# Kernel optimization log

Hardware: AMD Instinct MI355X
Metric: run time of the kernel (lower is better)

The kernel has to match this reference:

```python
import jax, jax.numpy as jnp
import numpy as np

EMBED_DIM = 1024
EXPAND_RATIO = 128  # head_dim; n_heads = EMBED_DIM // EXPAND_RATIO = 8
B, N = 4, 2048


def setup_inputs() -> dict:
    key = jax.random.key(0)
    ks = jax.random.split(key, 6)
    std = 0.02
    d = EMBED_DIM
    return {
        "x": jax.random.normal(ks[0], (B, N, d), dtype=jnp.float32),
        "Wq": jax.random.normal(ks[1], (d, d), dtype=jnp.float32) * std,
        "Wk": jax.random.normal(ks[2], (d, d), dtype=jnp.float32) * std,
        "Wv": jax.random.normal(ks[3], (d, d), dtype=jnp.float32) * std,
        "Wo": jax.random.normal(ks[4], (d, d), dtype=jnp.float32) * std,
        "norm_w": jnp.ones((d,), dtype=jnp.float32),
    }


def _rmsnorm(x, w, eps=1e-6):
    return x * jax.lax.rsqrt(jnp.mean(x * x, axis=-1, keepdims=True) + eps) * w


def _gla_scan(q, k, v, g):
    # q,k,v,g: [b, n, h, d]; state S: [b, h, d_k, d_v]
    b, n, h, d = q.shape
    qs, ks_, vs, gs = (jnp.moveaxis(t, 1, 0) for t in (q, k, v, g))  # [n,b,h,d]
    S0 = jnp.zeros((b, h, d, d), dtype=q.dtype)

    def step(S, inp):
        q_t, k_t, v_t, g_t = inp
        # S_t = diag(exp(g_t)) S_{t-1} + k_t^T v_t (gate on key dim)
        S = jnp.exp(g_t)[..., :, None] * S + k_t[..., :, None] * v_t[..., None, :]
        o_t = jnp.einsum('bhk,bhkv->bhv', q_t, S)
        return S, o_t

    _, outs = jax.lax.scan(step, S0, (qs, ks_, vs, gs))
    return jnp.moveaxis(outs, 0, 1)  # [b, n, h, d]


def reference(x, Wq, Wk, Wv, Wo, norm_w):
    b, n, D = x.shape
    hd = EXPAND_RATIO
    h = D // hd

    q = jax.nn.silu(x @ Wq.T)          # q_activation = silu
    f = jax.nn.sigmoid(x @ Wk.T)       # f = sigmoid(k_proj(x))
    log_f = jax.nn.log_sigmoid(f)      # faithful: logsigmoid applied to f (lower_bound=None path)
    k = 1.0 - f
    v = x @ Wv.T

    def split_heads(t):
        return t.reshape(b, n, h, hd)

    out = _gla_scan(split_heads(q), split_heads(k), split_heads(v), split_heads(log_f))
    out = out.reshape(b, n, D)
    out = _rmsnorm(out, norm_w)        # norm_pos='ogate', no output gate
    return out @ Wo.T
```

## Files before the change

### kernel.cpp

```cpp
#include <hip/hip_runtime.h>
#include <cstdint>
#include <cstddef>


typedef unsigned short u16;
using f32x4  = __attribute__((ext_vector_type(4))) float;
using bf16x8 = __attribute__((ext_vector_type(8))) short;

__device__ __forceinline__ float bf2f(u16 u) {
  union { unsigned int i; float f; } v; v.i = ((unsigned int)u) << 16; return v.f;
}
__device__ __forceinline__ u16 f2bf(float f) {
  union { float f; unsigned int i; } v; v.f = f;
  unsigned int r = v.i + 0x7fffu + ((v.i >> 16) & 1u);
  return (u16)(r >> 16);
}
__device__ __forceinline__ void async_load16(const void* g, void* l) {
  __builtin_amdgcn_global_load_lds(
      (const __attribute__((address_space(1))) unsigned int*)(uintptr_t)g,
      (__attribute__((address_space(3))) unsigned int*)(uintptr_t)l, 16, 0, 0);
}
__device__ __forceinline__ float logsig01(float f) {
  float u = f * f;
  return -0.69314718f + 0.5f * f + u * (-0.125f + u * (0.0052083335f - u * 3.472222e-4f));
}

__device__ __forceinline__ void gemm128_core(const u16* __restrict__ Ag, const u16* __restrict__ Bg,
                                             u16* smem, f32x4 (&acc)[4][4]) {
  const int tid = threadIdx.x;
  const int lane = tid & 63, wave = tid >> 6;
  const int wm = (wave & 1) * 64, wn = (wave >> 1) * 64;
  const int r = lane & 15, quad = lane >> 4;
  const int xk = r & 3;
  const u16* baseA = smem + (wm + r) * 32 + ((quad ^ xk) & 3) * 8;
  const u16* baseB = smem + 4096 + (wn + r) * 32 + ((quad ^ xk) & 3) * 8;
  const int soff = (tid >> 2) * 1024 + (((tid & 3) ^ ((tid >> 2) & 3)) * 8);
  u16* dA = smem + wave * 512;
  u16* dB = smem + 4096 + wave * 512;
#pragma unroll
  for (int it = 0; it < 2; ++it) {
    async_load16(Ag + it * 65536 + soff, dA + it * 2048);
    async_load16(Bg + it * 65536 + soff, dB + it * 2048);
  }
#pragma unroll 2
  for (int kt = 0; kt < 32; ++kt) {
    const int cb = (kt & 1) * 8192;
    __syncthreads();
    if (kt < 31) {
      const int nb = ((kt + 1) & 1) * 8192;
      const u16* As = Ag + (kt + 1) * 32 + soff;
      const u16* Bs = Bg + (kt + 1) * 32 + soff;
#pragma unroll
      for (int it = 0; it < 2; ++it) {
        async_load16(As + it * 65536, dA + nb + it * 2048);
        async_load16(Bs + it * 65536, dB + nb + it * 2048);
      }
    }
    bf16x8 af[4], bv[4];
#pragma unroll
    for (int i = 0; i < 4; ++i) af[i] = *(const bf16x8*)(baseA + cb + i * 512);
#pragma unroll
    for (int j = 0; j < 4; ++j) bv[j] = *(const bf16x8*)(baseB + cb + j * 512);
#pragma unroll
    for (int i = 0; i < 4; ++i)
#pragma unroll
      for (int j = 0; j < 4; ++j)
        acc[i][j] = __builtin_amdgcn_mfma_f32_16x16x32_bf16(af[i], bv[j], acc[i][j], 0, 0, 0);
  }
}

__global__ __launch_bounds__(256) void cast_all(
    const float* __restrict__ x, const float* __restrict__ w0, const float* __restrict__ w1,
    const float* __restrict__ w2, const float* __restrict__ w3, const float* __restrict__ nw,
    u16* __restrict__ xd, u16* __restrict__ d0, u16* __restrict__ d1,
    u16* __restrict__ d2, u16* __restrict__ d3) {
  const int blk = blockIdx.x;
  const float* src;
  u16* dst;
  int i;
  bool fold = false;
  if (blk < 8192) {
    src = x; dst = xd; i = blk * 256 + threadIdx.x;
  } else {
    int wb = blk - 8192, which = wb >> 10;
    i = (wb & 1023) * 256 + threadIdx.x;
    src = which == 0 ? w0 : (which == 1 ? w1 : (which == 2 ? w2 : w3));
    dst = which == 0 ? d0 : (which == 1 ? d1 : (which == 2 ? d2 : d3));
    fold = (which == 3);
  }
  float4 v = ((const float4*)src)[i];
  if (fold) {
    float4 wv = ((const float4*)nw)[i & 255];
    v.x *= wv.x; v.y *= wv.y; v.z *= wv.z; v.w *= wv.w;
  }
  unsigned int lo = (unsigned)f2bf(v.x) | ((unsigned)f2bf(v.y) << 16);
  unsigned int hi = (unsigned)f2bf(v.z) | ((unsigned)f2bf(v.w) << 16);
  ((uint2*)dst)[i] = make_uint2(lo, hi);
}

__global__ __launch_bounds__(256) void hgru_gemm_qkv(
    const u16* __restrict__ Xb, const u16* __restrict__ Wqb, const u16* __restrict__ Wkb,
    const u16* __restrict__ Wvb, u16* __restrict__ Qb, u16* __restrict__ Kb,
    u16* __restrict__ Vb) {
  __shared__ alignas(16) u16 smem[16384];
  const int which = blockIdx.y >> 3, bn = blockIdx.y & 7;
  const u16* W = which == 0 ? Wqb : (which == 1 ? Wkb : Wvb);
  const u16* Ag = Xb + (size_t)blockIdx.x * 128 * 1024;
  const u16* Bg = W + (size_t)bn * 128 * 1024;
  f32x4 acc[4][4] = {};
  gemm128_core(Ag, Bg, smem, acc);
  const int tid = threadIdx.x, lane = tid & 63, wave = tid >> 6;
  const int wm = (wave & 1) * 64, wn = (wave >> 1) * 64;
  const int r = lane & 15, quad = lane >> 4;
#pragma unroll
  for (int i = 0; i < 4; ++i)
#pragma unroll
    for (int j = 0; j < 4; ++j)
#pragma unroll
      for (int reg = 0; reg < 4; ++reg) {
        int m = blockIdx.x * 128 + wm + i * 16 + quad * 4 + reg;
        int n = bn * 128 + wn + j * 16 + r;
        size_t off = (size_t)m * 1024 + n;
        float z = acc[i][j][reg];
        if (which == 0) {
          Qb[off] = f2bf(z / (1.f + __expf(-z)));
        } else if (which == 1) {
          float ek = __expf(-z);
          Kb[off] = f2bf(ek / (1.f + ek));
        } else {
          Vb[off] = f2bf(z);
        }
      }
}

__global__ __launch_bounds__(256) void hgru_scan(
    const u16* __restrict__ Qg, const u16* __restrict__ Kg, const u16* __restrict__ Vg,
    u16* __restrict__ O, float* __restrict__ Ssum) {
  __shared__ alignas(16) char smem[42496];
  float* sb  = (float*)(smem);
  u16* sU    = (u16*)(smem);
  u16* sKt   = (u16*)(smem + 17408);
  u16* sVt1  = (u16*)(smem + 27648);
  u16* sQ    = (u16*)(smem + 17408);
  u16* sK    = (u16*)(smem + 26112);
  u16* sVt2  = (u16*)(smem + 34816);
  u16* sAm   = (u16*)(smem + 39936);

  const int tid = threadIdx.x, blk = blockIdx.x;
  const int vh = blk & 1, c = (blk >> 1) & 63, bh = blk >> 7, h = bh & 7, bb_ = bh >> 3;
  const size_t rb = (size_t)(bb_ * 2048 + c * 32) * 1024 + h * 128;
  const bool haveP = (c > 0);
  const size_t rb1 = haveP ? rb - 32 * 1024 : rb;

  const int lane = tid & 63, wave = tid >> 6;
  const int r = lane & 15, quad = lane >> 4;
  const int ts = tid & 31;
  const int g8 = tid >> 5;

  uint4 Q2[2], K2[2], K1[2], V2, V1;
#pragma unroll
  for (int it = 0; it < 2; ++it) {
    Q2[it] = *(const uint4*)(Qg + rb  + (size_t)ts * 1024 + (it * 8 + g8) * 8);
    K2[it] = *(const uint4*)(Kg + rb  + (size_t)ts * 1024 + (it * 8 + g8) * 8);
    K1[it] = *(const uint4*)(Kg + rb1 + (size_t)ts * 1024 + (it * 8 + g8) * 8);
  }
  V2 = *(const uint4*)(Vg + rb  + (size_t)ts * 1024 + vh * 64 + g8 * 8);
  V1 = *(const uint4*)(Vg + rb1 + (size_t)ts * 1024 + vh * 64 + g8 * 8);

  f32x4 accU[2][4] = {};
  const int vm = (wave & 1) * 32, in = (wave >> 1) * 64;

  if (haveP) {
    { const int col = tid & 127, half = tid >> 7;
      float run = 0.f;
      const size_t gb = rb1 + (size_t)(half * 16) * 1024 + col;
#pragma unroll
      for (int t = 0; t < 16; ++t) {
        float kv = bf2f(Kg[gb + (size_t)t * 1024]);
        run += logsig01(1.f - kv);
        sb[(half * 16 + t) * 129 + col] = run;
      } }
    __syncthreads();
    { if (tid >> 7) { const int col = tid & 127; float fix = sb[15 * 129 + col];
#pragma unroll
        for (int t = 16; t < 32; ++t) sb[t * 129 + col] += fix; } }
    __syncthreads();
#pragma unroll
    for (int it = 0; it < 2; ++it) {
      const int i8 = it * 8 + g8;
      const u16* kp = (const u16*)&K1[it];
#pragma unroll
      for (int e = 0; e < 8; ++e) {
        int i = i8 * 8 + e;
        float bs = sb[ts * 129 + i];
        float bC = sb[31 * 129 + i];
        sKt[i * 40 + ts] = f2bf(bf2f(kp[e]) * __expf(bC - bs));
      }
    }
    { const u16* vp = (const u16*)&V1;
#pragma unroll
      for (int e = 0; e < 8; ++e) sVt1[(g8 * 8 + e) * 40 + ts] = vp[e]; }
    __syncthreads();
#pragma unroll
    for (int mi = 0; mi < 2; ++mi) {
      bf16x8 af = *(const bf16x8*)(sVt1 + (vm + mi * 16 + r) * 40 + quad * 8);
#pragma unroll
      for (int nj = 0; nj < 4; ++nj) {
        bf16x8 bv = *(const bf16x8*)(sKt + (in + nj * 16 + r) * 40 + quad * 8);
        accU[mi][nj] = __builtin_amdgcn_mfma_f32_16x16x32_bf16(af, bv, accU[mi][nj], 0, 0, 0);
      }
    }
  }
  { const int col = tid & 127, half = tid >> 7;
    float run = 0.f;
    const size_t gb = rb + (size_t)(half * 16) * 1024 + col;
#pragma unroll
    for (int t = 0; t < 16; ++t) {
      float kv = bf2f(Kg[gb + (size_t)t * 1024]);
      run += logsig01(1.f - kv);
      sb[(half * 16 + t) * 129 + col] = run;
    } }
  __syncthreads();
  { if (tid >> 7) { const int col = tid & 127; float fix = sb[15 * 129 + col];
#pragma unroll
      for (int t = 16; t < 32; ++t) sb[t * 129 + col] += fix; } }
  __syncthreads();
#pragma unroll
  for (int it = 0; it < 2; ++it) {
    const int i8 = it * 8 + g8;
    const u16* qp = (const u16*)&Q2[it];
    const u16* kp = (const u16*)&K2[it];
    u16 qo[8], ko[8];
#pragma unroll
    for (int e = 0; e < 8; ++e) {
      int i = i8 * 8 + e;
      float bt = sb[ts * 129 + i];
      qo[e] = f2bf(bf2f(qp[e]) * __expf(bt));
      ko[e] = f2bf(bf2f(kp[e]) * __expf(-bt));
    }
    *(uint4*)(sQ + ts * 136 + i8 * 8) = *(const uint4*)qo;
    *(uint4*)(sK + ts * 136 + i8 * 8) = *(const uint4*)ko;
  }
  { const u16* vp = (const u16*)&V2;
#pragma unroll
    for (int e = 0; e < 8; ++e) sVt2[(g8 * 8 + e) * 40 + ts] = vp[e]; }
  __syncthreads();
  { const int mi = wave & 1, nj = wave >> 1;
    f32x4 a1 = {0.f, 0.f, 0.f, 0.f};
#pragma unroll
    for (int ks = 0; ks < 4; ++ks) {
      bf16x8 af = *(const bf16x8*)(sQ + (mi * 16 + r) * 136 + ks * 32 + quad * 8);
      bf16x8 bk = *(const bf16x8*)(sK + (nj * 16 + r) * 136 + ks * 32 + quad * 8);
      a1 = __builtin_amdgcn_mfma_f32_16x16x32_bf16(af, bk, a1, 0, 0, 0);
    }
#pragma unroll
    for (int reg = 0; reg < 4; ++reg) {
      int t = mi * 16 + quad * 4 + reg, s = nj * 16 + r;
      sAm[t * 40 + s] = (s <= t) ? f2bf(a1[reg]) : (u16)0;
    } }
  if (haveP) {
#pragma unroll
    for (int mi = 0; mi < 2; ++mi)
#pragma unroll
      for (int nj = 0; nj < 4; ++nj)
#pragma unroll
        for (int reg = 0; reg < 4; ++reg) {
          int vl = vm + mi * 16 + quad * 4 + reg;
          int i  = in + nj * 16 + r;
          sU[vl * 136 + i] = f2bf(accU[mi][nj][reg]);
        }
  }
  __syncthreads();
  { const int mi = wave & 1, no = (wave >> 1) * 32;
    bf16x8 af0 = *(const bf16x8*)(sAm + (mi * 16 + r) * 40 + quad * 8);
    bf16x8 afq[4];
    if (haveP) {
#pragma unroll
      for (int ks = 0; ks < 4; ++ks)
        afq[ks] = *(const bf16x8*)(sQ + (mi * 16 + r) * 136 + ks * 32 + quad * 8);
    }
    f32x4 ssq = {0.f, 0.f, 0.f, 0.f};
#pragma unroll
    for (int j = 0; j < 2; ++j) {
      f32x4 acc2 = {0.f, 0.f, 0.f, 0.f};
      bf16x8 bv0 = *(const bf16x8*)(sVt2 + (no + j * 16 + r) * 40 + quad * 8);
      acc2 = __builtin_amdgcn_mfma_f32_16x16x32_bf16(af0, bv0, acc2, 0, 0, 0);
      if (haveP) {
#pragma unroll
        for (int ks = 0; ks < 4; ++ks) {
          bf16x8 bs = *(const bf16x8*)(sU + (no + j * 16 + r) * 136 + ks * 32 + quad * 8);
          acc2 = __builtin_amdgcn_mfma_f32_16x16x32_bf16(afq[ks], bs, acc2, 0, 0, 0);
        }
      }
      ssq += acc2 * acc2;
#pragma unroll
      for (int reg = 0; reg < 4; ++reg) {
        int t = mi * 16 + quad * 4 + reg;
        int vg = vh * 64 + no + j * 16 + r;
        O[rb + (size_t)t * 1024 + vg] = f2bf(acc2[reg]);
      }
    }
    const int rowg = bb_ * 2048 + c * 32 + mi * 16 + quad * 4;
#pragma unroll
    for (int reg = 0; reg < 4; ++reg) {
      float v = ssq[reg];
      v += __shfl_xor(v, 1); v += __shfl_xor(v, 2);
      v += __shfl_xor(v, 4); v += __shfl_xor(v, 8);
      if (r == 0) atomicAdd(&Ssum[rowg + reg], v);
    } }
}

__global__ __launch_bounds__(256) void hgru_gemm_out(const u16* __restrict__ Ab,
                                                     const u16* __restrict__ Wob,
                                                     const float* __restrict__ Ssum,
                                                     float* __restrict__ out) {
  __shared__ alignas(16) u16 smem[16384];
  const u16* Ag = Ab + (size_t)blockIdx.x * 128 * 1024;
  const u16* Bg = Wob + (size_t)blockIdx.y * 128 * 1024;
  f32x4 acc[4][4] = {};
  gemm128_core(Ag, Bg, smem, acc);
  const int tid = threadIdx.x, lane = tid & 63, wave = tid >> 6;
  const int wm = (wave & 1) * 64, wn = (wave >> 1) * 64;
  const int r = lane & 15, quad = lane >> 4;
#pragma unroll
  for (int i = 0; i < 4; ++i)
#pragma unroll
    for (int reg = 0; reg < 4; ++reg) {
      int m = blockIdx.x * 128 + wm + i * 16 + quad * 4 + reg;
      float sm = rsqrtf(Ssum[m] * (1.f / 1024.f) + 1e-6f);
#pragma unroll
      for (int j = 0; j < 4; ++j) {
        int n = blockIdx.y * 128 + wn + j * 16 + r;
        out[(size_t)m * 1024 + n] = acc[i][j][reg] * sm;
      }
    }
}

extern "C" void kernel_launch(void* const* d_in, const int* in_sizes, int n_in,
                              void* d_out, int out_size, void* d_ws, size_t ws_size,
                              hipStream_t stream) {
  const float* x  = (const float*)d_in[0];
  const float* Wq = (const float*)d_in[1];
  const float* Wk = (const float*)d_in[2];
  const float* Wv = (const float*)d_in[3];
  const float* Wo = (const float*)d_in[4];
  const float* nw = (const float*)d_in[5];
  float* out = (float*)d_out;
  char* ws = (char*)d_ws;

  u16* Xb   = (u16*)(ws + 0);
  u16* Wqb  = (u16*)(ws + 16777216);
  u16* Wkb  = (u16*)(ws + 18874368);
  u16* Wvb  = (u16*)(ws + 20971520);
  u16* Wob  = (u16*)(ws + 23068672);
  u16* Qb   = (u16*)(ws + 25165824);
  u16* Kb   = (u16*)(ws + 41943040);
  u16* Vb   = (u16*)(ws + 58720256);
  u16* Obf  = (u16*)(ws + 75497472);
  float* Sv = (float*)(ws + 92274688);

  cast_all<<<12288, 256, 0, stream>>>(x, Wq, Wk, Wv, Wo, nw, Xb, Wqb, Wkb, Wvb, Wob);
  hipMemsetAsync(Sv, 0, 8192 * sizeof(float), stream);

  dim3 gq(64, 24);
  hgru_gemm_qkv<<<gq, 256, 0, stream>>>(Xb, Wqb, Wkb, Wvb, Qb, Kb, Vb);
  hgru_scan<<<4096, 256, 0, stream>>>(Qb, Kb, Vb, Obf, Sv);
  dim3 go(64, 8);
  hgru_gemm_out<<<go, 256, 0, stream>>>(Obf, Wob, Sv, out);
}
```

Before: 238.3 us.

## Restructure scan chunk prologue to cut barriers and stage output via LDS

Each scan block now computes the gate cumulative sum with one serial pass per column instead of a two-half scan held in shared memory. Half the threads handle the previous chunk's decayed K and the other half the current chunk's Q/K, which removes several __syncthreads and the float prefix buffer. The output tile is staged in LDS and written back with coalesced 16-byte stores, launch bounds request 4 blocks per CU, and the Ssum memset is folded into the cast kernel. In exchange, the serial 32-step loops lengthen per-thread latency and the per-column global loads are scalar 2-byte reads.

```diff
diff --git a/kernel.cpp b/kernel.cpp
--- a/kernel.cpp
+++ b/kernel.cpp
@@ -73,8 +73,12 @@
     const float* __restrict__ x, const float* __restrict__ w0, const float* __restrict__ w1,
     const float* __restrict__ w2, const float* __restrict__ w3, const float* __restrict__ nw,
     u16* __restrict__ xd, u16* __restrict__ d0, u16* __restrict__ d1,
-    u16* __restrict__ d2, u16* __restrict__ d3) {
+    u16* __restrict__ d2, u16* __restrict__ d3, float* __restrict__ Sv) {
   const int blk = blockIdx.x;
+  if (blk >= 12288) {
+    Sv[(blk - 12288) * 256 + threadIdx.x] = 0.f;
+    return;
+  }
   const float* src;
   u16* dst;
   int i;
@@ -133,18 +137,18 @@
       }
 }
 
-__global__ __launch_bounds__(256) void hgru_scan(
+__global__ __launch_bounds__(256, 4) void hgru_scan(
     const u16* __restrict__ Qg, const u16* __restrict__ Kg, const u16* __restrict__ Vg,
     u16* __restrict__ O, float* __restrict__ Ssum) {
-  __shared__ alignas(16) char smem[42496];
-  float* sb  = (float*)(smem);
-  u16* sU    = (u16*)(smem);
-  u16* sKt   = (u16*)(smem + 17408);
-  u16* sVt1  = (u16*)(smem + 27648);
-  u16* sQ    = (u16*)(smem + 17408);
-  u16* sK    = (u16*)(smem + 26112);
-  u16* sVt2  = (u16*)(smem + 34816);
-  u16* sAm   = (u16*)(smem + 39936);
+  __shared__ alignas(16) char smem[40448];
+  u16* sKt  = (u16*)(smem);
+  u16* sVt1 = (u16*)(smem + 10240);
+  u16* sK   = (u16*)(smem + 15360);
+  u16* sQ   = (u16*)(smem + 24064);
+  u16* sVt2 = (u16*)(smem + 32768);
+  u16* sAm  = (u16*)(smem + 37888);
+  u16* sU   = (u16*)(smem);
+  u16* sO   = (u16*)(smem + 17408);
 
   const int tid = threadIdx.x, blk = blockIdx.x;
   const int vh = blk & 1, c = (blk >> 1) & 63, bh = blk >> 7, h = bh & 7, bb_ = bh >> 3;
@@ -154,53 +158,62 @@
 
   const int lane = tid & 63, wave = tid >> 6;
   const int r = lane & 15, quad = lane >> 4;
-  const int ts = tid & 31;
-  const int g8 = tid >> 5;
-
-  uint4 Q2[2], K2[2], K1[2], V2, V1;
-#pragma unroll
-  for (int it = 0; it < 2; ++it) {
-    Q2[it] = *(const uint4*)(Qg + rb  + (size_t)ts * 1024 + (it * 8 + g8) * 8);
-    K2[it] = *(const uint4*)(Kg + rb  + (size_t)ts * 1024 + (it * 8 + g8) * 8);
-    K1[it] = *(const uint4*)(Kg + rb1 + (size_t)ts * 1024 + (it * 8 + g8) * 8);
-  }
-  V2 = *(const uint4*)(Vg + rb  + (size_t)ts * 1024 + vh * 64 + g8 * 8);
-  V1 = *(const uint4*)(Vg + rb1 + (size_t)ts * 1024 + vh * 64 + g8 * 8);
+  const int ts = tid & 31, g8 = tid >> 5;
+
+  uint4 V2 = *(const uint4*)(Vg + rb  + (size_t)ts * 1024 + vh * 64 + g8 * 8);
+  uint4 V1 = *(const uint4*)(Vg + rb1 + (size_t)ts * 1024 + vh * 64 + g8 * 8);
+  { const u16* vp = (const u16*)&V2;
+#pragma unroll
+    for (int e = 0; e < 8; ++e) sVt2[(g8 * 8 + e) * 40 + ts] = vp[e]; }
+  if (haveP) {
+    const u16* vp = (const u16*)&V1;
+#pragma unroll
+    for (int e = 0; e < 8; ++e) sVt1[(g8 * 8 + e) * 40 + ts] = vp[e];
+  }
+
+  const int col = tid & 127;
+  if (tid < 128) {
+    if (haveP) {
+      const u16* kc = Kg + rb1 + col;
+      unsigned int kraw[16];
+      float bC = 0.f;
+#pragma unroll
+      for (int t = 0; t < 16; ++t) {
+        unsigned int a = kc[(size_t)(2 * t) * 1024];
+        unsigned int b = kc[(size_t)(2 * t + 1) * 1024];
+        kraw[t] = a | (b << 16);
+        bC += logsig01(1.f - bf2f((u16)a)) + logsig01(1.f - bf2f((u16)b));
+      }
+      float run = 0.f;
+#pragma unroll
+      for (int t = 0; t < 16; ++t) {
+        float ka = bf2f((u16)(kraw[t] & 0xffff));
+        float kb = bf2f((u16)(kraw[t] >> 16));
+        run += logsig01(1.f - ka);
+        sKt[col * 40 + 2 * t]     = f2bf(ka * __expf(bC - run));
+        run += logsig01(1.f - kb);
+        sKt[col * 40 + 2 * t + 1] = f2bf(kb * __expf(bC - run));
+      }
+    }
+  } else {
+    const u16* kc = Kg + rb + col;
+    const u16* qc = Qg + rb + col;
+    float run = 0.f;
+#pragma unroll
+    for (int t = 0; t < 32; ++t) {
+      u16 ku = kc[(size_t)t * 1024];
+      u16 qu = qc[(size_t)t * 1024];
+      float kv = bf2f(ku);
+      run += logsig01(1.f - kv);
+      sQ[t * 136 + col] = f2bf(bf2f(qu) * __expf(run));
+      sK[t * 136 + col] = f2bf(kv * __expf(-run));
+    }
+  }
+  __syncthreads();
 
   f32x4 accU[2][4] = {};
   const int vm = (wave & 1) * 32, in = (wave >> 1) * 64;
-
   if (haveP) {
-    { const int col = tid & 127, half = tid >> 7;
-      float run = 0.f;
-      const size_t gb = rb1 + (size_t)(half * 16) * 1024 + col;
-#pragma unroll
-      for (int t = 0; t < 16; ++t) {
-        float kv = bf2f(Kg[gb + (size_t)t * 1024]);
-        run += logsig01(1.f - kv);
-        sb[(half * 16 + t) * 129 + col] = run;
-      } }
-    __syncthreads();
-    { if (tid >> 7) { const int col = tid & 127; float fix = sb[15 * 129 + col];
-#pragma unroll
-        for (int t = 16; t < 32; ++t) sb[t * 129 + col] += fix; } }
-    __syncthreads();
-#pragma unroll
-    for (int it = 0; it < 2; ++it) {
-      const int i8 = it * 8 + g8;
-      const u16* kp = (const u16*)&K1[it];
-#pragma unroll
-      for (int e = 0; e < 8; ++e) {
-        int i = i8 * 8 + e;
-        float bs = sb[ts * 129 + i];
-        float bC = sb[31 * 129 + i];
-        sKt[i * 40 + ts] = f2bf(bf2f(kp[e]) * __expf(bC - bs));
-      }
-    }
-    { const u16* vp = (const u16*)&V1;
-#pragma unroll
-      for (int e = 0; e < 8; ++e) sVt1[(g8 * 8 + e) * 40 + ts] = vp[e]; }
-    __syncthreads();
 #pragma unroll
     for (int mi = 0; mi < 2; ++mi) {
       bf16x8 af = *(const bf16x8*)(sVt1 + (vm + mi * 16 + r) * 40 + quad * 8);
@@ -211,40 +224,6 @@
       }
     }
   }
-  { const int col = tid & 127, half = tid >> 7;
-    float run = 0.f;
-    const size_t gb = rb + (size_t)(half * 16) * 1024 + col;
-#pragma unroll
-    for (int t = 0; t < 16; ++t) {
-      float kv = bf2f(Kg[gb + (size_t)t * 1024]);
-      run += logsig01(1.f - kv);
-      sb[(half * 16 + t) * 129 + col] = run;
-    } }
-  __syncthreads();
-  { if (tid >> 7) { const int col = tid & 127; float fix = sb[15 * 129 + col];
-#pragma unroll
-      for (int t = 16; t < 32; ++t) sb[t * 129 + col] += fix; } }
-  __syncthreads();
-#pragma unroll
-  for (int it = 0; it < 2; ++it) {
-    const int i8 = it * 8 + g8;
-    const u16* qp = (const u16*)&Q2[it];
-    const u16* kp = (const u16*)&K2[it];
-    u16 qo[8], ko[8];
-#pragma unroll
-    for (int e = 0; e < 8; ++e) {
-      int i = i8 * 8 + e;
-      float bt = sb[ts * 129 + i];
-      qo[e] = f2bf(bf2f(qp[e]) * __expf(bt));
-      ko[e] = f2bf(bf2f(kp[e]) * __expf(-bt));
-    }
-    *(uint4*)(sQ + ts * 136 + i8 * 8) = *(const uint4*)qo;
-    *(uint4*)(sK + ts * 136 + i8 * 8) = *(const uint4*)ko;
-  }
-  { const u16* vp = (const u16*)&V2;
-#pragma unroll
-    for (int e = 0; e < 8; ++e) sVt2[(g8 * 8 + e) * 40 + ts] = vp[e]; }
-  __syncthreads();
   { const int mi = wave & 1, nj = wave >> 1;
     f32x4 a1 = {0.f, 0.f, 0.f, 0.f};
 #pragma unroll
@@ -258,6 +237,8 @@
       int t = mi * 16 + quad * 4 + reg, s = nj * 16 + r;
       sAm[t * 40 + s] = (s <= t) ? f2bf(a1[reg]) : (u16)0;
     } }
+  __syncthreads();
+
   if (haveP) {
 #pragma unroll
     for (int mi = 0; mi < 2; ++mi)
@@ -271,6 +252,7 @@
         }
   }
   __syncthreads();
+
   { const int mi = wave & 1, no = (wave >> 1) * 32;
     bf16x8 af0 = *(const bf16x8*)(sAm + (mi * 16 + r) * 40 + quad * 8);
     bf16x8 afq[4];
@@ -296,8 +278,7 @@
 #pragma unroll
       for (int reg = 0; reg < 4; ++reg) {
         int t = mi * 16 + quad * 4 + reg;
-        int vg = vh * 64 + no + j * 16 + r;
-        O[rb + (size_t)t * 1024 + vg] = f2bf(acc2[reg]);
+        sO[t * 72 + no + j * 16 + r] = f2bf(acc2[reg]);
       }
     }
     const int rowg = bb_ * 2048 + c * 32 + mi * 16 + quad * 4;
@@ -308,6 +289,11 @@
       v += __shfl_xor(v, 4); v += __shfl_xor(v, 8);
       if (r == 0) atomicAdd(&Ssum[rowg + reg], v);
     } }
+  __syncthreads();
+
+  { const int row = tid >> 3, seg = tid & 7;
+    *(uint4*)(O + rb + (size_t)row * 1024 + vh * 64 + seg * 8) =
+        *(const uint4*)(sO + row * 72 + seg * 8); }
 }
 
 __global__ __launch_bounds__(256) void hgru_gemm_out(const u16* __restrict__ Ab,
@@ -359,8 +345,7 @@
   u16* Obf  = (u16*)(ws + 75497472);
   float* Sv = (float*)(ws + 92274688);
 
-  cast_all<<<12288, 256, 0, stream>>>(x, Wq, Wk, Wv, Wo, nw, Xb, Wqb, Wkb, Wvb, Wob);
-  hipMemsetAsync(Sv, 0, 8192 * sizeof(float), stream);
+  cast_all<<<12320, 256, 0, stream>>>(x, Wq, Wk, Wv, Wo, nw, Xb, Wqb, Wkb, Wvb, Wob, Sv);
 
   dim3 gq(64, 24);
   hgru_gemm_qkv<<<gq, 256, 0, stream>>>(Xb, Wqb, Wkb, Wvb, Qb, Kb, Vb);
```

Result: faster. 228.6 us (-4.1%).
